# Kernel tuning notes

Measured on AMD Instinct MI355X. Metric: run time of the kernel, lower is better.

The kernel has to match this reference:

```python
import jax, jax.numpy as jnp
import numpy as np

IN_F, OUT_F, RANK = 4096, 4096, 64
B, S = 4, 2048


def setup_inputs() -> dict:
    key = jax.random.key(0)
    k1, k2, k3 = jax.random.split(key, 3)
    x = jax.random.normal(k1, (B, S, IN_F), dtype=jnp.float32)
    # Low-rank compressed weight factors: W = U @ V^T, shape [OUT_F, IN_F]
    U = jax.random.normal(k2, (OUT_F, RANK), dtype=jnp.float32) / np.sqrt(RANK)
    V = jax.random.normal(k3, (IN_F, RANK), dtype=jnp.float32) / np.sqrt(IN_F)
    bias = jnp.zeros((OUT_F,), dtype=jnp.float32)
    return {"x": x, "U": U, "V": V, "bias": bias}


def reference(x, U, V, bias):
    # Decompress: weight = compressor.decompress(compressed_weight) -> [out, in]
    weight = jnp.einsum("or,ir->oi", U, V)  # materialized like the original
    # F.linear(x, weight, bias) = x @ weight^T + bias
    return jnp.einsum("bsi,oi->bso", x, weight) + bias
```

## Files before the change

### kernel.cpp

```cpp
#include <hip/hip_runtime.h>

#define IN_F    4096
#define OUT_F   4096
#define RANK    64
#define M_TOTAL 8192
#define M_TILE  16
#define BLOCK   512
#define NWAVES  8
#define KSPLIT  4

using short8  = __attribute__((ext_vector_type(8))) short;
using float4v = __attribute__((ext_vector_type(4))) float;

#define MFMA16(A, B, C) __builtin_amdgcn_mfma_f32_16x16x32_bf16((A), (B), (C), 0, 0, 0)

__device__ __forceinline__ void split2(float x, short& h, short& l) {
    unsigned u = __float_as_uint(x);
    unsigned t = u & 0xffff0000u;
    h = (short)(t >> 16);
    float r = x - __uint_as_float(t);
    l = (short)(__float_as_uint(r) >> 16);
}

__device__ __forceinline__ void split_f4x2(float4 a, float4 b, short8& hi, short8& lo) {
    short h0,h1,h2,h3,h4,h5,h6,h7, l0,l1,l2,l3,l4,l5,l6,l7;
    split2(a.x,h0,l0); split2(a.y,h1,l1); split2(a.z,h2,l2); split2(a.w,h3,l3);
    split2(b.x,h4,l4); split2(b.y,h5,l5); split2(b.z,h6,l6); split2(b.w,h7,l7);
    hi = (short8){h0,h1,h2,h3,h4,h5,h6,h7};
    lo = (short8){l0,l1,l2,l3,l4,l5,l6,l7};
}


__global__ void prep_uv(const float* __restrict__ V, const float* __restrict__ U,
                        unsigned short* __restrict__ vt_hi, unsigned short* __restrict__ vt_lo,
                        unsigned short* __restrict__ u_hi,  unsigned short* __restrict__ u_lo)
{
    const int b = blockIdx.x;
    const int linear = (b & 255) * 256 + threadIdx.x;
    short h[4], l[4];
    if (b < 256) {
        const int r  = linear >> 10;
        const int k0 = (linear & 1023) * 4;
        #pragma unroll
        for (int i = 0; i < 4; ++i)
            split2(V[(size_t)(k0 + i) * RANK + r], h[i], l[i]);
        const size_t o = (size_t)r * IN_F + k0;
        *(ushort4*)(vt_hi + o) = make_ushort4((unsigned short)h[0], (unsigned short)h[1],
                                              (unsigned short)h[2], (unsigned short)h[3]);
        *(ushort4*)(vt_lo + o) = make_ushort4((unsigned short)l[0], (unsigned short)l[1],
                                              (unsigned short)l[2], (unsigned short)l[3]);
    } else {
        const int idx = linear * 4;
        const float4 u4 = *(const float4*)(U + idx);
        split2(u4.x, h[0], l[0]); split2(u4.y, h[1], l[1]);
        split2(u4.z, h[2], l[2]); split2(u4.w, h[3], l[3]);
        *(ushort4*)(u_hi + idx) = make_ushort4((unsigned short)h[0], (unsigned short)h[1],
                                               (unsigned short)h[2], (unsigned short)h[3]);
        *(ushort4*)(u_lo + idx) = make_ushort4((unsigned short)l[0], (unsigned short)l[1],
                                               (unsigned short)l[2], (unsigned short)l[3]);
    }
}

__global__ __launch_bounds__(256, 2) void lowrank_xv4(
    const float* __restrict__ x,
    const unsigned short* __restrict__ vt_hi, const unsigned short* __restrict__ vt_lo,
    float* __restrict__ t_part)
{
    __shared__ float part[KSPLIT][64][RANK + 4];

    const int tid  = threadIdx.x;
    const int wv   = tid >> 6;
    const int lane = tid & 63;
    const int l15  = lane & 15;
    const int quad = lane >> 4;
    const int kq   = blockIdx.x & 3;
    const int mg   = blockIdx.x >> 2;
    const int m0   = mg * 64;
    const int kbase = kq * 1024 + wv * 256;

    float4v acc[4][4] = {};
    const float* xp[4];
    #pragma unroll
    for (int mf = 0; mf < 4; ++mf)
        xp[mf] = x + (size_t)(m0 + mf * 16 + l15) * IN_F + kbase + quad * 8;
    const unsigned short* vh = vt_hi + (size_t)l15 * IN_F + kbase + quad * 8;
    const unsigned short* vl = vt_lo + (size_t)l15 * IN_F + kbase + quad * 8;

    float4 xa[4], xb[4];
    short8 bh[4], bl[4];
    #pragma unroll
    for (int mf = 0; mf < 4; ++mf) {
        xa[mf] = *(const float4*)(xp[mf]);
        xb[mf] = *(const float4*)(xp[mf] + 4);
    }
    #pragma unroll
    for (int rt = 0; rt < 4; ++rt) {
        bh[rt] = *(const short8*)(vh + (size_t)rt * 16 * IN_F);
        bl[rt] = *(const short8*)(vl + (size_t)rt * 16 * IN_F);
    }

    #pragma unroll
    for (int ks = 0; ks < 8; ++ks) {
        const int kn = (ks + 1) * 32;
        float4 na[4], nb[4];
        short8 nh[4], nl[4];
        #pragma unroll
        for (int mf = 0; mf < 4; ++mf) {
            na[mf] = xa[mf]; nb[mf] = xb[mf];
            if (ks < 7) {
                na[mf] = *(const float4*)(xp[mf] + kn);
                nb[mf] = *(const float4*)(xp[mf] + kn + 4);
            }
        }
        #pragma unroll
        for (int rt = 0; rt < 4; ++rt) {
            nh[rt] = bh[rt]; nl[rt] = bl[rt];
            if (ks < 7) {
                nh[rt] = *(const short8*)(vh + (size_t)rt * 16 * IN_F + kn);
                nl[rt] = *(const short8*)(vl + (size_t)rt * 16 * IN_F + kn);
            }
        }
        #pragma unroll
        for (int mf = 0; mf < 4; ++mf) {
            short8 a_hi, a_lo;
            split_f4x2(xa[mf], xb[mf], a_hi, a_lo);
            #pragma unroll
            for (int rt = 0; rt < 4; ++rt) {
                acc[mf][rt] = MFMA16(a_lo, bh[rt], acc[mf][rt]);
                acc[mf][rt] = MFMA16(a_hi, bl[rt], acc[mf][rt]);
                acc[mf][rt] = MFMA16(a_hi, bh[rt], acc[mf][rt]);
            }
        }
        #pragma unroll
        for (int mf = 0; mf < 4; ++mf) { xa[mf] = na[mf]; xb[mf] = nb[mf]; }
        #pragma unroll
        for (int rt = 0; rt < 4; ++rt) { bh[rt] = nh[rt]; bl[rt] = nl[rt]; }
    }

    #pragma unroll
    for (int mf = 0; mf < 4; ++mf)
        #pragma unroll
        for (int rt = 0; rt < 4; ++rt)
            #pragma unroll
            for (int rg = 0; rg < 4; ++rg)
                part[wv][mf * 16 + quad * 4 + rg][rt * 16 + l15] = acc[mf][rt][rg];
    __syncthreads();

    {
        const int e  = tid * 16;
        const int m  = e >> 6;
        const int r0 = e & 63;
        float* dst = t_part + (size_t)kq * (M_TOTAL * RANK)
                   + (size_t)(m0 + m) * RANK + r0;
        #pragma unroll
        for (int j = 0; j < 4; ++j) {
            float4 s = {0.f, 0.f, 0.f, 0.f};
            #pragma unroll
            for (int p = 0; p < KSPLIT; ++p) {
                const float4 v = *(const float4*)(&part[p][m][r0 + j * 4]);
                s.x += v.x; s.y += v.y; s.z += v.z; s.w += v.w;
            }
            *(float4*)(dst + j * 4) = s;
        }
    }
}

__global__ __launch_bounds__(256, 3) void lowrank_tu4(
    const float* __restrict__ t_part,
    const unsigned short* __restrict__ u_hi, const unsigned short* __restrict__ u_lo,
    const float* __restrict__ bias, float* __restrict__ out)
{
    const int tid  = threadIdx.x;
    const int wv   = tid >> 6;
    const int lane = tid & 63;
    const int l15  = lane & 15;
    const int quad = lane >> 4;
    const int og   = blockIdx.x & 31;
    const int mg   = blockIdx.x >> 5;
    const int m0   = mg * 256 + wv * 64;
    const int o0   = og * 128;

    short8 ta_hi[4][2], ta_lo[4][2];
    #pragma unroll
    for (int mf = 0; mf < 4; ++mf) {
        const float* tp = t_part + (size_t)(m0 + mf * 16 + l15) * RANK + quad * 8;
        float4 s0 = *(const float4*)(tp);
        float4 s1 = *(const float4*)(tp + 4);
        float4 s2 = *(const float4*)(tp + 32);
        float4 s3 = *(const float4*)(tp + 36);
        #pragma unroll
        for (int p = 1; p < KSPLIT; ++p) {
            const float* q = tp + (size_t)p * (M_TOTAL * RANK);
            const float4 a0 = *(const float4*)(q);
            const float4 a1 = *(const float4*)(q + 4);
            const float4 a2 = *(const float4*)(q + 32);
            const float4 a3 = *(const float4*)(q + 36);
            s0.x += a0.x; s0.y += a0.y; s0.z += a0.z; s0.w += a0.w;
            s1.x += a1.x; s1.y += a1.y; s1.z += a1.z; s1.w += a1.w;
            s2.x += a2.x; s2.y += a2.y; s2.z += a2.z; s2.w += a2.w;
            s3.x += a3.x; s3.y += a3.y; s3.z += a3.z; s3.w += a3.w;
        }
        split_f4x2(s0, s1, ta_hi[mf][0], ta_lo[mf][0]);
        split_f4x2(s2, s3, ta_hi[mf][1], ta_lo[mf][1]);
    }

    const unsigned short* up_h = u_hi + (size_t)(o0 + l15) * RANK + quad * 8;
    const unsigned short* up_l = u_lo + (size_t)(o0 + l15) * RANK + quad * 8;
    short8 uh0 = *(const short8*)(up_h), uh1 = *(const short8*)(up_h + 32);
    short8 ul0 = *(const short8*)(up_l), ul1 = *(const short8*)(up_l + 32);

    #pragma unroll
    for (int nt = 0; nt < 8; ++nt) {
        short8 nh0 = uh0, nh1 = uh1, nl0 = ul0, nl1 = ul1;
        if (nt < 7) {
            const int adv = (nt + 1) * 16 * RANK;
            nh0 = *(const short8*)(up_h + adv);   nh1 = *(const short8*)(up_h + adv + 32);
            nl0 = *(const short8*)(up_l + adv);   nl1 = *(const short8*)(up_l + adv + 32);
        }
        const int o = o0 + nt * 16 + l15;
        const float bv = bias[o];
        #pragma unroll
        for (int mf = 0; mf < 4; ++mf) {
            float4v acc = {bv, bv, bv, bv};
            acc = MFMA16(ta_lo[mf][0], uh0, acc);
            acc = MFMA16(ta_hi[mf][0], ul0, acc);
            acc = MFMA16(ta_hi[mf][0], uh0, acc);
            acc = MFMA16(ta_lo[mf][1], uh1, acc);
            acc = MFMA16(ta_hi[mf][1], ul1, acc);
            acc = MFMA16(ta_hi[mf][1], uh1, acc);
            float* op = out + (size_t)(m0 + mf * 16 + quad * 4) * OUT_F + o;
            op[0 * OUT_F] = acc[0];
            op[1 * OUT_F] = acc[1];
            op[2 * OUT_F] = acc[2];
            op[3 * OUT_F] = acc[3];
        }
        uh0 = nh0; uh1 = nh1; ul0 = nl0; ul1 = nl1;
    }
}


__global__ __launch_bounds__(BLOCK, 4) void lowrank_xv(
    const float* __restrict__ x,
    const unsigned short* __restrict__ vt_hi, const unsigned short* __restrict__ vt_lo,
    unsigned short* __restrict__ t_hi, unsigned short* __restrict__ t_lo)
{
    __shared__ float part[NWAVES][M_TILE][RANK + 4];

    const int tid  = threadIdx.x;
    const int wv   = tid >> 6;
    const int lane = tid & 63;
    const int l15  = lane & 15;
    const int quad = lane >> 4;
    const int m0   = blockIdx.x * M_TILE;

    float4v acc[4] = {};
    const float*          xp = x     + (size_t)(m0 + l15) * IN_F + wv * 512 + quad * 8;
    const unsigned short* vh = vt_hi + (size_t)l15 * IN_F + wv * 512 + quad * 8;
    const unsigned short* vl = vt_lo + (size_t)l15 * IN_F + wv * 512 + quad * 8;

    float4 xa = *(const float4*)(xp);
    float4 xb = *(const float4*)(xp + 4);
    #pragma unroll
    for (int ks = 0; ks < 16; ++ks) {
        const int k0 = ks * 32;
        float4 na = xa, nb = xb;
        if (ks < 15) {
            na = *(const float4*)(xp + k0 + 32);
            nb = *(const float4*)(xp + k0 + 36);
        }
        short8 a_hi, a_lo;
        split_f4x2(xa, xb, a_hi, a_lo);
        #pragma unroll
        for (int rt = 0; rt < 4; ++rt) {
            short8 b_hi = *(const short8*)(vh + (size_t)rt * 16 * IN_F + k0);
            short8 b_lo = *(const short8*)(vl + (size_t)rt * 16 * IN_F + k0);
            acc[rt] = MFMA16(a_lo, b_hi, acc[rt]);
            acc[rt] = MFMA16(a_hi, b_lo, acc[rt]);
            acc[rt] = MFMA16(a_hi, b_hi, acc[rt]);
        }
        xa = na; xb = nb;
    }

    #pragma unroll
    for (int rt = 0; rt < 4; ++rt)
        #pragma unroll
        for (int rg = 0; rg < 4; ++rg)
            part[wv][quad * 4 + rg][rt * 16 + l15] = acc[rt][rg];
    __syncthreads();

    const int e = tid * 2;
    const int m = e >> 6, r = e & 63;
    float s0 = 0.f, s1 = 0.f;
    #pragma unroll
    for (int w = 0; w < NWAVES; ++w) { s0 += part[w][m][r]; s1 += part[w][m][r + 1]; }
    short h0, l0, h1, l1;
    split2(s0, h0, l0); split2(s1, h1, l1);
    const size_t off = (size_t)m0 * RANK + e;
    *(ushort2*)(t_hi + off) = make_ushort2((unsigned short)h0, (unsigned short)h1);
    *(ushort2*)(t_lo + off) = make_ushort2((unsigned short)l0, (unsigned short)l1);
}

__global__ __launch_bounds__(256, 4) void lowrank_tu(
    const unsigned short* __restrict__ t_hi, const unsigned short* __restrict__ t_lo,
    const unsigned short* __restrict__ u_hi, const unsigned short* __restrict__ u_lo,
    const float* __restrict__ bias, float* __restrict__ out)
{
    const int tid  = threadIdx.x;
    const int wv   = tid >> 6;
    const int lane = tid & 63;
    const int l15  = lane & 15;
    const int quad = lane >> 4;
    const int og   = blockIdx.x & 7;
    const int mg   = blockIdx.x >> 3;
    const int m0   = mg * 64 + wv * 16;
    const int o0   = og * 512;

    short8 ta_hi[2], ta_lo[2];
    {
        const unsigned short* tp_h = t_hi + (size_t)(m0 + l15) * RANK + quad * 8;
        const unsigned short* tp_l = t_lo + (size_t)(m0 + l15) * RANK + quad * 8;
        ta_hi[0] = *(const short8*)(tp_h);   ta_hi[1] = *(const short8*)(tp_h + 32);
        ta_lo[0] = *(const short8*)(tp_l);   ta_lo[1] = *(const short8*)(tp_l + 32);
    }

    #pragma unroll 2
    for (int nt = 0; nt < 32; ++nt) {
        const int o = o0 + nt * 16 + l15;
        const unsigned short* up_h = u_hi + (size_t)o * RANK + quad * 8;
        const unsigned short* up_l = u_lo + (size_t)o * RANK + quad * 8;
        const float bv = bias[o];
        float4v acc = {bv, bv, bv, bv};
        #pragma unroll
        for (int ks = 0; ks < 2; ++ks) {
            short8 uh = *(const short8*)(up_h + ks * 32);
            short8 ul = *(const short8*)(up_l + ks * 32);
            acc = MFMA16(ta_lo[ks], uh, acc);
            acc = MFMA16(ta_hi[ks], ul, acc);
            acc = MFMA16(ta_hi[ks], uh, acc);
        }
        float* op = out + (size_t)(m0 + quad * 4) * OUT_F + o;
        op[0 * OUT_F] = acc[0];
        op[1 * OUT_F] = acc[1];
        op[2 * OUT_F] = acc[2];
        op[3 * OUT_F] = acc[3];
    }
}

__global__ __launch_bounds__(256, 2) void fallback_fp32(
    const float* __restrict__ x, const float* __restrict__ U,
    const float* __restrict__ V, const float* __restrict__ bias,
    float* __restrict__ out)
{
    __shared__ float v_lds[128][RANK];
    __shared__ float t_lds[8][RANK];
    const int tid = threadIdx.x, lane = tid & 63, wave = tid >> 6;
    const int m0 = blockIdx.x * 8;
    float acc0 = 0.f, acc1 = 0.f;
    const size_t row_base = (size_t)(m0 + wave * 2) * IN_F;
    for (int kt = 0; kt < IN_F; kt += 128) {
        const float4* Vg = (const float4*)(V + (size_t)kt * RANK);
        float4* Vs = (float4*)(&v_lds[0][0]);
        #pragma unroll
        for (int i = 0; i < 8; ++i) Vs[tid + 256 * i] = Vg[tid + 256 * i];
        __syncthreads();
        const float* xp = x + row_base + kt;
        #pragma unroll 8
        for (int k = 0; k < 128; k += 4) {
            float v0 = v_lds[k+0][lane], v1 = v_lds[k+1][lane];
            float v2 = v_lds[k+2][lane], v3 = v_lds[k+3][lane];
            float4 xa = *(const float4*)(xp + 0 * IN_F + k);
            float4 xb = *(const float4*)(xp + 1 * IN_F + k);
            acc0 += xa.x*v0 + xa.y*v1 + xa.z*v2 + xa.w*v3;
            acc1 += xb.x*v0 + xb.y*v1 + xb.z*v2 + xb.w*v3;
        }
        __syncthreads();
    }
    t_lds[wave*2+0][lane] = acc0;
    t_lds[wave*2+1][lane] = acc1;
    __syncthreads();
    for (int oc = 0; oc < OUT_F; oc += 1024) {
        const int o4 = oc + tid * 4;
        const float4 b4 = *(const float4*)(bias + o4);
        float4 a0=b4,a1=b4,a2=b4,a3=b4,a4=b4,a5=b4,a6=b4,a7=b4;
        const float* Up = U + (size_t)o4 * RANK;
        #pragma unroll 2
        for (int r0 = 0; r0 < RANK; r0 += 4) {
            const float4 u0 = *(const float4*)(Up + 0*RANK + r0);
            const float4 u1 = *(const float4*)(Up + 1*RANK + r0);
            const float4 u2 = *(const float4*)(Up + 2*RANK + r0);
            const float4 u3 = *(const float4*)(Up + 3*RANK + r0);
            #define P2_STEP(AM, MM) { \
                const float4 t4 = *(const float4*)(&t_lds[MM][r0]); \
                AM.x += t4.x*u0.x + t4.y*u0.y + t4.z*u0.z + t4.w*u0.w; \
                AM.y += t4.x*u1.x + t4.y*u1.y + t4.z*u1.z + t4.w*u1.w; \
                AM.z += t4.x*u2.x + t4.y*u2.y + t4.z*u2.z + t4.w*u2.w; \
                AM.w += t4.x*u3.x + t4.y*u3.y + t4.z*u3.z + t4.w*u3.w; }
            P2_STEP(a0,0) P2_STEP(a1,1) P2_STEP(a2,2) P2_STEP(a3,3)
            P2_STEP(a4,4) P2_STEP(a5,5) P2_STEP(a6,6) P2_STEP(a7,7)
            #undef P2_STEP
        }
        float* op = out + (size_t)m0 * OUT_F + o4;
        *(float4*)(op+0*OUT_F)=a0; *(float4*)(op+1*OUT_F)=a1;
        *(float4*)(op+2*OUT_F)=a2; *(float4*)(op+3*OUT_F)=a3;
        *(float4*)(op+4*OUT_F)=a4; *(float4*)(op+5*OUT_F)=a5;
        *(float4*)(op+6*OUT_F)=a6; *(float4*)(op+7*OUT_F)=a7;
    }
}

extern "C" void kernel_launch(void* const* d_in, const int* in_sizes, int n_in,
                              void* d_out, int out_size, void* d_ws, size_t ws_size,
                              hipStream_t stream) {
    const float* x    = (const float*)d_in[0];
    const float* U    = (const float*)d_in[1];
    const float* V    = (const float*)d_in[2];
    const float* bias = (const float*)d_in[3];
    float* out = (float*)d_out;

    const size_t E = (size_t)RANK * IN_F;
    const size_t T = (size_t)M_TOTAL * RANK;
    const size_t need_v5 = (E * 4) * sizeof(unsigned short)
                         + (size_t)KSPLIT * T * sizeof(float);
    const size_t need_v2 = (E * 4 + T * 2) * sizeof(unsigned short);

    if (ws_size >= need_v5) {
        unsigned short* vt_hi = (unsigned short*)d_ws;
        unsigned short* vt_lo = vt_hi + E;
        unsigned short* u_hi  = vt_lo + E;
        unsigned short* u_lo  = u_hi  + E;
        float*          t_part = (float*)(u_lo + E);
        prep_uv<<<dim3(512), dim3(256), 0, stream>>>(V, U, vt_hi, vt_lo, u_hi, u_lo);
        lowrank_xv4<<<dim3((M_TOTAL / 64) * KSPLIT), dim3(256), 0, stream>>>(
            x, vt_hi, vt_lo, t_part);
        lowrank_tu4<<<dim3((M_TOTAL / 256) * (OUT_F / 128)), dim3(256), 0, stream>>>(
            t_part, u_hi, u_lo, bias, out);
    } else if (ws_size >= need_v2) {
        unsigned short* vt_hi = (unsigned short*)d_ws;
        unsigned short* vt_lo = vt_hi + E;
        unsigned short* u_hi  = vt_lo + E;
        unsigned short* u_lo  = u_hi  + E;
        unsigned short* t_hi  = u_lo  + E;
        unsigned short* t_lo  = t_hi  + T;
        prep_uv<<<dim3(512), dim3(256), 0, stream>>>(V, U, vt_hi, vt_lo, u_hi, u_lo);
        lowrank_xv<<<dim3(M_TOTAL / M_TILE), dim3(BLOCK), 0, stream>>>(
            x, vt_hi, vt_lo, t_hi, t_lo);
        lowrank_tu<<<dim3((M_TOTAL / 64) * (OUT_F / 512)), dim3(256), 0, stream>>>(
            t_hi, t_lo, u_hi, u_lo, bias, out);
    } else {
        fallback_fp32<<<dim3(M_TOTAL / 8), dim3(256), 0, stream>>>(x, U, V, bias, out);
    }
}
```

Before: 320.8 us.

## Stage x and V tiles through double-buffered LDS in the projection kernel

The x·V kernel now uses 512-thread blocks that cooperatively load 64x32 x tiles and V hi/lo tiles into double-buffered shared memory. Each wave computes a 16x32 sub-tile over the full 1024-wide K chunk, so the cross-wave LDS reduction is gone and V fragments are shared across waves instead of each wave loading its own from global. The second kernel halves rows per wave (32 instead of 64), which doubles the grid and raises the occupancy hint. The cost is a __syncthreads on every K step and fewer MFMAs per LDS read, which may reduce arithmetic intensity.

```diff
diff --git a/kernel.cpp b/kernel.cpp
--- a/kernel.cpp
+++ b/kernel.cpp
@@ -61,111 +61,79 @@
     }
 }
 
-__global__ __launch_bounds__(256, 2) void lowrank_xv4(
+__global__ __launch_bounds__(512, 4) void lowrank_xv5(
     const float* __restrict__ x,
     const unsigned short* __restrict__ vt_hi, const unsigned short* __restrict__ vt_lo,
     float* __restrict__ t_part)
 {
-    __shared__ float part[KSPLIT][64][RANK + 4];
+    __shared__ float          xs[2][64][36];
+    __shared__ unsigned short vs[2][2][64][40];
 
     const int tid  = threadIdx.x;
     const int wv   = tid >> 6;
     const int lane = tid & 63;
     const int l15  = lane & 15;
     const int quad = lane >> 4;
+    const int msub = wv >> 1;
+    const int rsub = wv & 1;
     const int kq   = blockIdx.x & 3;
     const int mg   = blockIdx.x >> 2;
     const int m0   = mg * 64;
-    const int kbase = kq * 1024 + wv * 256;
-
-    float4v acc[4][4] = {};
-    const float* xp[4];
-    #pragma unroll
-    for (int mf = 0; mf < 4; ++mf)
-        xp[mf] = x + (size_t)(m0 + mf * 16 + l15) * IN_F + kbase + quad * 8;
-    const unsigned short* vh = vt_hi + (size_t)l15 * IN_F + kbase + quad * 8;
-    const unsigned short* vl = vt_lo + (size_t)l15 * IN_F + kbase + quad * 8;
-
-    float4 xa[4], xb[4];
-    short8 bh[4], bl[4];
-    #pragma unroll
-    for (int mf = 0; mf < 4; ++mf) {
-        xa[mf] = *(const float4*)(xp[mf]);
-        xb[mf] = *(const float4*)(xp[mf] + 4);
-    }
-    #pragma unroll
-    for (int rt = 0; rt < 4; ++rt) {
-        bh[rt] = *(const short8*)(vh + (size_t)rt * 16 * IN_F);
-        bl[rt] = *(const short8*)(vl + (size_t)rt * 16 * IN_F);
-    }
-
-    #pragma unroll
-    for (int ks = 0; ks < 8; ++ks) {
-        const int kn = (ks + 1) * 32;
-        float4 na[4], nb[4];
-        short8 nh[4], nl[4];
-        #pragma unroll
-        for (int mf = 0; mf < 4; ++mf) {
-            na[mf] = xa[mf]; nb[mf] = xb[mf];
-            if (ks < 7) {
-                na[mf] = *(const float4*)(xp[mf] + kn);
-                nb[mf] = *(const float4*)(xp[mf] + kn + 4);
-            }
-        }
-        #pragma unroll
-        for (int rt = 0; rt < 4; ++rt) {
-            nh[rt] = bh[rt]; nl[rt] = bl[rt];
-            if (ks < 7) {
-                nh[rt] = *(const short8*)(vh + (size_t)rt * 16 * IN_F + kn);
-                nl[rt] = *(const short8*)(vl + (size_t)rt * 16 * IN_F + kn);
-            }
-        }
-        #pragma unroll
-        for (int mf = 0; mf < 4; ++mf) {
-            short8 a_hi, a_lo;
-            split_f4x2(xa[mf], xb[mf], a_hi, a_lo);
-            #pragma unroll
-            for (int rt = 0; rt < 4; ++rt) {
-                acc[mf][rt] = MFMA16(a_lo, bh[rt], acc[mf][rt]);
-                acc[mf][rt] = MFMA16(a_hi, bl[rt], acc[mf][rt]);
-                acc[mf][rt] = MFMA16(a_hi, bh[rt], acc[mf][rt]);
-            }
-        }
-        #pragma unroll
-        for (int mf = 0; mf < 4; ++mf) { xa[mf] = na[mf]; xb[mf] = nb[mf]; }
-        #pragma unroll
-        for (int rt = 0; rt < 4; ++rt) { bh[rt] = nh[rt]; bl[rt] = nl[rt]; }
-    }
-
-    #pragma unroll
-    for (int mf = 0; mf < 4; ++mf)
-        #pragma unroll
-        for (int rt = 0; rt < 4; ++rt)
-            #pragma unroll
-            for (int rg = 0; rg < 4; ++rg)
-                part[wv][mf * 16 + quad * 4 + rg][rt * 16 + l15] = acc[mf][rt][rg];
+    const int kbase = kq * 1024;
+
+    const int sxr = tid >> 3, sxc = (tid & 7) * 4;
+    const int svp = tid >> 8;
+    const int svr = (tid & 255) >> 2, svc = (tid & 3) * 8;
+    const float*          xg = x + (size_t)(m0 + sxr) * IN_F + kbase + sxc;
+    const unsigned short* vg = (svp ? vt_lo : vt_hi) + (size_t)svr * IN_F + kbase + svc;
+
+    {
+        float4 x0 = *(const float4*)(xg);
+        short8 v0 = *(const short8*)(vg);
+        *(float4*)(&xs[0][sxr][sxc]) = x0;
+        *(short8*)(&vs[0][svp][svr][svc]) = v0;
+    }
     __syncthreads();
 
-    {
-        const int e  = tid * 16;
-        const int m  = e >> 6;
-        const int r0 = e & 63;
-        float* dst = t_part + (size_t)kq * (M_TOTAL * RANK)
-                   + (size_t)(m0 + m) * RANK + r0;
-        #pragma unroll
-        for (int j = 0; j < 4; ++j) {
-            float4 s = {0.f, 0.f, 0.f, 0.f};
-            #pragma unroll
-            for (int p = 0; p < KSPLIT; ++p) {
-                const float4 v = *(const float4*)(&part[p][m][r0 + j * 4]);
-                s.x += v.x; s.y += v.y; s.z += v.z; s.w += v.w;
-            }
-            *(float4*)(dst + j * 4) = s;
-        }
-    }
-}
-
-__global__ __launch_bounds__(256, 3) void lowrank_tu4(
+    float4v acc[2] = {};
+    for (int ks = 0; ks < 32; ++ks) {
+        const int cur = ks & 1;
+        float4 nx = {0.f, 0.f, 0.f, 0.f};
+        short8 nv = {};
+        if (ks < 31) {
+            nx = *(const float4*)(xg + (ks + 1) * 32);
+            nv = *(const short8*)(vg + (ks + 1) * 32);
+        }
+        float4 xa = *(const float4*)(&xs[cur][msub * 16 + l15][quad * 8]);
+        float4 xb = *(const float4*)(&xs[cur][msub * 16 + l15][quad * 8 + 4]);
+        short8 a_hi, a_lo;
+        split_f4x2(xa, xb, a_hi, a_lo);
+        #pragma unroll
+        for (int rt = 0; rt < 2; ++rt) {
+            const int rr = rsub * 32 + rt * 16 + l15;
+            short8 bhv = *(const short8*)(&vs[cur][0][rr][quad * 8]);
+            short8 blv = *(const short8*)(&vs[cur][1][rr][quad * 8]);
+            acc[rt] = MFMA16(a_lo, bhv, acc[rt]);
+            acc[rt] = MFMA16(a_hi, blv, acc[rt]);
+            acc[rt] = MFMA16(a_hi, bhv, acc[rt]);
+        }
+        if (ks < 31) {
+            *(float4*)(&xs[cur ^ 1][sxr][sxc]) = nx;
+            *(short8*)(&vs[cur ^ 1][svp][svr][svc]) = nv;
+        }
+        __syncthreads();
+    }
+
+    float* base = t_part + (size_t)kq * (M_TOTAL * RANK);
+    #pragma unroll
+    for (int rt = 0; rt < 2; ++rt)
+        #pragma unroll
+        for (int rg = 0; rg < 4; ++rg)
+            base[(size_t)(m0 + msub * 16 + quad * 4 + rg) * RANK
+                 + rsub * 32 + rt * 16 + l15] = acc[rt][rg];
+}
+
+__global__ __launch_bounds__(256, 4) void lowrank_tu5(
     const float* __restrict__ t_part,
     const unsigned short* __restrict__ u_hi, const unsigned short* __restrict__ u_lo,
     const float* __restrict__ bias, float* __restrict__ out)
@@ -177,12 +145,12 @@
     const int quad = lane >> 4;
     const int og   = blockIdx.x & 31;
     const int mg   = blockIdx.x >> 5;
-    const int m0   = mg * 256 + wv * 64;
+    const int m0   = mg * 128 + wv * 32;
     const int o0   = og * 128;
 
-    short8 ta_hi[4][2], ta_lo[4][2];
-    #pragma unroll
-    for (int mf = 0; mf < 4; ++mf) {
+    short8 ta_hi[2][2], ta_lo[2][2];
+    #pragma unroll
+    for (int mf = 0; mf < 2; ++mf) {
         const float* tp = t_part + (size_t)(m0 + mf * 16 + l15) * RANK + quad * 8;
         float4 s0 = *(const float4*)(tp);
         float4 s1 = *(const float4*)(tp + 4);
@@ -220,7 +188,7 @@
         const int o = o0 + nt * 16 + l15;
         const float bv = bias[o];
         #pragma unroll
-        for (int mf = 0; mf < 4; ++mf) {
+        for (int mf = 0; mf < 2; ++mf) {
             float4v acc = {bv, bv, bv, bv};
             acc = MFMA16(ta_lo[mf][0], uh0, acc);
             acc = MFMA16(ta_hi[mf][0], ul0, acc);
@@ -418,20 +386,20 @@
 
     const size_t E = (size_t)RANK * IN_F;
     const size_t T = (size_t)M_TOTAL * RANK;
-    const size_t need_v5 = (E * 4) * sizeof(unsigned short)
+    const size_t need_v6 = (E * 4) * sizeof(unsigned short)
                          + (size_t)KSPLIT * T * sizeof(float);
     const size_t need_v2 = (E * 4 + T * 2) * sizeof(unsigned short);
 
-    if (ws_size >= need_v5) {
+    if (ws_size >= need_v6) {
         unsigned short* vt_hi = (unsigned short*)d_ws;
         unsigned short* vt_lo = vt_hi + E;
         unsigned short* u_hi  = vt_lo + E;
         unsigned short* u_lo  = u_hi  + E;
         float*          t_part = (float*)(u_lo + E);
         prep_uv<<<dim3(512), dim3(256), 0, stream>>>(V, U, vt_hi, vt_lo, u_hi, u_lo);
-        lowrank_xv4<<<dim3((M_TOTAL / 64) * KSPLIT), dim3(256), 0, stream>>>(
+        lowrank_xv5<<<dim3((M_TOTAL / 64) * KSPLIT), dim3(512), 0, stream>>>(
             x, vt_hi, vt_lo, t_part);
-        lowrank_tu4<<<dim3((M_TOTAL / 256) * (OUT_F / 128)), dim3(256), 0, stream>>>(
+        lowrank_tu5<<<dim3((M_TOTAL / 128) * (OUT_F / 128)), dim3(256), 0, stream>>>(
             t_part, u_hi, u_lo, bias, out);
     } else if (ws_size >= need_v2) {
         unsigned short* vt_hi = (unsigned short*)d_ws;
```

Result: faster. 303.5 us (-5.4%).
